# Kernel optimization log

Measured on AMD Instinct MI355X. Metric: run time of the kernel, lower is better.

## Reference

```python
import jax, jax.numpy as jnp
import numpy as np
import math

D = 512  # feature dim (must equal Lv for the final bmm)

def setup_inputs() -> dict:
    key = jax.random.key(0)
    k1, k2, k3 = jax.random.split(key, 3)
    B, Lp, Lq, Lv = 32, 1024, 1024, 512
    linear_pre = jax.random.normal(k1, (B, Lp, D), dtype=jnp.float32)
    linear_q = jax.random.normal(k2, (B, Lq, D), dtype=jnp.float32)
    linear_v = jax.random.normal(k3, (B, Lv, D), dtype=jnp.float32)
    return {"linear_pre": linear_pre, "linear_q": linear_q, "linear_v": linear_v}

def reference(linear_pre, linear_q, linear_v):
    scale = 1.0 / math.sqrt(D)
    # Two parallel softmax-attention streams (exp / sum == softmax over last dim).
    # attnp: [B, Lp, Lq], attne: [B, Lq, Lv]
    attnp = jax.nn.softmax(jnp.einsum('bpd,bqd->bpq', linear_pre, linear_q) * scale, axis=-1)
    attne = jax.nn.softmax(jnp.einsum('bqd,bvd->bqv', linear_q, linear_v) * scale, axis=-1)
    # dropout is identity in eval mode (deterministic reference)
    precompute = jnp.einsum('bpq,bqd->bpd', attnp, linear_q)   # [B, Lp, D]
    energy = jnp.einsum('bqv,bvd->bqd', attne, linear_v)       # [B, Lq, D]
    # final bmm requires D == Lv
    weightedContext = jnp.einsum('bqv,bvd->bqd', energy, linear_v)  # [B, Lq, D]
    return (weightedContext, energy, precompute)
```

## Files before the change

### kernel.cpp

```cpp
#include <hip/hip_runtime.h>

#define BATCH 32
#define LP 1024
#define LQ 1024
#define LV 512
#define DIM 512

typedef __bf16 bf16x8 __attribute__((ext_vector_type(8)));
typedef float f32x4 __attribute__((ext_vector_type(4)));
typedef unsigned short ushort_t;
typedef unsigned short us8 __attribute__((ext_vector_type(8)));

__device__ __forceinline__ ushort_t f2bf(float f) {
  unsigned int u = __float_as_uint(f);
  unsigned int r = (u + 0x7FFFu + ((u >> 16) & 1u)) >> 16;
  return (ushort_t)r;
}

__device__ __forceinline__ void async16(const void* g, void* l) {
  __builtin_amdgcn_global_load_lds(
      (const __attribute__((address_space(1))) unsigned int*)g,
      (__attribute__((address_space(3))) unsigned int*)l, 16, 0, 0);
}

#define BARRIER() asm volatile("s_barrier" ::: "memory")
#define VMCNT(n) asm volatile("s_waitcnt vmcnt(" #n ")" ::: "memory")

__global__ __launch_bounds__(256)
void cvt_kernel(const float* __restrict__ in, ushort_t* __restrict__ out) {
  int i = blockIdx.x * blockDim.x + threadIdx.x;
  const float4* p = (const float4*)in;
  float4 a = p[i * 2], b = p[i * 2 + 1];
  us8 h;
  h[0] = f2bf(a.x); h[1] = f2bf(a.y); h[2] = f2bf(a.z); h[3] = f2bf(a.w);
  h[4] = f2bf(b.x); h[5] = f2bf(b.y); h[6] = f2bf(b.z); h[7] = f2bf(b.w);
  *(us8*)&out[(size_t)i * 8] = h;
}

__global__ void transpose_cvt(const float* __restrict__ in, ushort_t* __restrict__ outT,
                              ushort_t* __restrict__ outR, int R, int C) {
  __shared__ ushort_t tile[32][33];
  int b = blockIdx.z;
  int c0 = blockIdx.x * 32, r0 = blockIdx.y * 32;
  const float* inb = in + (size_t)b * R * C;
  ushort_t* outTb = outT + (size_t)b * R * C;
  ushort_t* outRb = outR + (size_t)b * R * C;
  int x = threadIdx.x, y = threadIdx.y;
#pragma unroll
  for (int k = 0; k < 4; ++k) {
    int r = r0 + y + k * 8;
    ushort_t h = f2bf(inb[(size_t)r * C + c0 + x]);
    tile[y + k * 8][x] = h;
    outRb[(size_t)r * C + c0 + x] = h;
  }
  __syncthreads();
#pragma unroll
  for (int k = 0; k < 4; ++k) {
    int c = c0 + y + k * 8;
    outTb[(size_t)c * R + r0 + x] = tile[x][y + k * 8];
  }
}

template <int H>
__device__ __forceinline__ void mm8(f32x4 (&acc)[8][4], const bf16x8 (&af)[4],
                                    const bf16x8 (&bfv)[4]) {
  __builtin_amdgcn_s_setprio(1);
#pragma unroll
  for (int i = 0; i < 4; ++i)
#pragma unroll
    for (int j = 0; j < 4; ++j)
      acc[H * 4 + i][j] =
          __builtin_amdgcn_mfma_f32_16x16x32_bf16(af[i], bfv[j], acc[H * 4 + i][j], 0, 0, 0);
  __builtin_amdgcn_s_setprio(0);
}

template <int MODE, bool OUT2>
__global__ __launch_bounds__(512, 2)
void gemm256(const ushort_t* __restrict__ A, const ushort_t* __restrict__ BT,
             const float* __restrict__ lsumIn, float* __restrict__ outF,
             ushort_t* __restrict__ outB, float* __restrict__ lsumOut,
             int M, int N, int K) {
  extern __shared__ ushort_t smem[];
  ushort_t* sA = smem;
  ushort_t* sB = smem + 32768;

  int b = blockIdx.z;
  int m0 = blockIdx.x * 256, n0 = blockIdx.y * 256;
  const ushort_t* Ab = A + ((size_t)b * M + m0) * K;
  const ushort_t* Bb = BT + ((size_t)b * N + n0) * K;
  int tid = threadIdx.x;
  int l = tid & 63, w = tid >> 6;
  int wm = w >> 2, wn = w & 3;
  int low = l & 15, quad = l >> 4;
  const int colsw = (quad * 8) ^ ((l & 8) ? 16 : 0);

  int NT = K >> 6;

  f32x4 acc[8][4];
  f32x4 zero = {0.f, 0.f, 0.f, 0.f};
#pragma unroll
  for (int i = 0; i < 8; ++i)
#pragma unroll
    for (int j = 0; j < 4; ++j) acc[i][j] = zero;

  auto stageT = [&](const ushort_t* gb, ushort_t* sbase, int T, int kh) {
    ushort_t* hb = sbase + (((T & 1) << 1) + kh) * 8192;
    int kc0 = (T << 6) + (kh << 5);
#pragma unroll
    for (int ii = 0; ii < 2; ++ii) {
      int o = w * 128 + ii * 64;
      int ol = o + l;
      int cc = ((ol & 3) ^ ((l >> 4) & 2)) << 3;
      async16(gb + (size_t)(ol >> 2) * K + kc0 + cc, hb + o * 8);
    }
  };
  auto ldA = [&](bf16x8 (&af)[4], int buf, int k, int h) {
    const ushort_t* base = sA + ((buf << 1) + k) * 8192 + colsw;
    int r0 = wm * 128 + h * 64 + low;
#pragma unroll
    for (int i = 0; i < 4; ++i) af[i] = *(const bf16x8*)&base[(r0 + i * 16) * 32];
  };
  auto ldB = [&](bf16x8 (&bfv)[4], int buf, int k) {
    const ushort_t* base = sB + ((buf << 1) + k) * 8192 + colsw;
    int r0 = wn * 64 + low;
#pragma unroll
    for (int j = 0; j < 4; ++j) bfv[j] = *(const bf16x8*)&base[(r0 + j * 16) * 32];
  };

  stageT(Ab, sA, 0, 0);
  stageT(Bb, sB, 0, 0);
  stageT(Ab, sA, 0, 1);
  stageT(Bb, sB, 0, 1);
  VMCNT(4);
  if (NT > 1) {
    stageT(Bb, sB, 1, 0);
    stageT(Ab, sA, 1, 0);
    stageT(Bb, sB, 1, 1);
    VMCNT(6);
  } else {
    VMCNT(0);
  }
  BARRIER();

  bf16x8 af[4], bfv[4];
  for (int T = 0; T < NT; ++T) {
    int buf = T & 1;
    ldB(bfv, buf, 0);
    ldA(af, buf, 0, 0);
    if (T + 1 < NT) stageT(Ab, sA, T + 1, 1);
    BARRIER();
    mm8<0>(acc, af, bfv);
    BARRIER();
    ldA(af, buf, 0, 1);
    if (T + 2 < NT) stageT(Bb, sB, T + 2, 0);
    BARRIER();
    mm8<1>(acc, af, bfv);
    BARRIER();
    ldB(bfv, buf, 1);
    ldA(af, buf, 1, 0);
    if (T + 2 < NT) stageT(Ab, sA, T + 2, 0);
    BARRIER();
    mm8<0>(acc, af, bfv);
    BARRIER();
    ldA(af, buf, 1, 1);
    if (T + 2 < NT) stageT(Bb, sB, T + 2, 1);
    if (T + 1 < NT) {
      if (T + 2 < NT) { VMCNT(6); } else { VMCNT(0); }
    }
    BARRIER();
    mm8<1>(acc, af, bfv);
    BARRIER();
  }

  size_t ob = (size_t)b * M * N;
  if (MODE == 2) {
    const float sc = 0.04419417382415922f;
#pragma unroll
    for (int i = 0; i < 8; ++i) {
      int gr0 = m0 + wm * 128 + i * 16 + quad * 4;
#pragma unroll
      for (int r = 0; r < 4; ++r) {
        int gr = gr0 + r;
        float rs = 0.f;
#pragma unroll
        for (int j = 0; j < 4; ++j) {
          float p = __expf(acc[i][j][r] * sc);
          rs += p;
          int gc = n0 + wn * 64 + j * 16 + low;
          outB[ob + (size_t)gr * N + gc] = f2bf(p);
        }
        rs += __shfl_xor(rs, 1);
        rs += __shfl_xor(rs, 2);
        rs += __shfl_xor(rs, 4);
        rs += __shfl_xor(rs, 8);
        if (low == 0) atomicAdd(&lsumOut[(size_t)b * M + gr], rs);
      }
    }
  } else {
#pragma unroll
    for (int i = 0; i < 8; ++i) {
      int gr0 = m0 + wm * 128 + i * 16 + quad * 4;
#pragma unroll
      for (int r = 0; r < 4; ++r) {
        int gr = gr0 + r;
        float inv = 1.f;
        if (MODE == 1) inv = 1.f / lsumIn[(size_t)b * M + gr];
#pragma unroll
        for (int j = 0; j < 4; ++j) {
          int gc = n0 + wn * 64 + j * 16 + low;
          float o = acc[i][j][r] * inv;
          outF[ob + (size_t)gr * N + gc] = o;
          if (OUT2) outB[ob + (size_t)gr * N + gc] = f2bf(o);
        }
      }
    }
  }
}

#define LDS_BYTES 131072

extern "C" void kernel_launch(void* const* d_in, const int* in_sizes, int n_in,
                              void* d_out, int out_size, void* d_ws, size_t ws_size,
                              hipStream_t stream) {
  (void)in_sizes; (void)n_in; (void)out_size; (void)ws_size;
  const float* pre = (const float*)d_in[0];
  const float* q   = (const float*)d_in[1];
  const float* v   = (const float*)d_in[2];

  float* out      = (float*)d_out;
  float* wc       = out;
  float* energy   = out + (size_t)BATCH * LQ * DIM;
  float* precomp  = out + 2 * (size_t)BATCH * LQ * DIM;

  char* ws = (char*)d_ws;
  size_t off = 0;
  auto alloc = [&](size_t bytes) {
    void* p = ws + off;
    off += (bytes + 255) & ~(size_t)255;
    return p;
  };
  ushort_t* preB = (ushort_t*)alloc((size_t)BATCH * LP * DIM * 2);
  ushort_t* qB   = (ushort_t*)alloc((size_t)BATCH * LQ * DIM * 2);
  ushort_t* vB   = (ushort_t*)alloc((size_t)BATCH * LV * DIM * 2);
  ushort_t* qT   = (ushort_t*)alloc((size_t)BATCH * DIM * LQ * 2);
  ushort_t* vT   = (ushort_t*)alloc((size_t)BATCH * DIM * LV * 2);
  ushort_t* Pp   = (ushort_t*)alloc((size_t)BATCH * LP * LQ * 2);
  ushort_t* Pe   = (ushort_t*)alloc((size_t)BATCH * LQ * LV * 2);
  ushort_t* Ebf  = (ushort_t*)alloc((size_t)BATCH * LQ * DIM * 2);
  float* lp = (float*)alloc((size_t)BATCH * LP * 4);
  float* le = (float*)alloc((size_t)BATCH * LQ * 4);

  static bool attr_done = false;
  if (!attr_done) {
    attr_done = true;
    hipFuncSetAttribute(reinterpret_cast<const void*>(&gemm256<2, false>),
                        hipFuncAttributeMaxDynamicSharedMemorySize, LDS_BYTES);
    hipFuncSetAttribute(reinterpret_cast<const void*>(&gemm256<1, false>),
                        hipFuncAttributeMaxDynamicSharedMemorySize, LDS_BYTES);
    hipFuncSetAttribute(reinterpret_cast<const void*>(&gemm256<1, true>),
                        hipFuncAttributeMaxDynamicSharedMemorySize, LDS_BYTES);
    hipFuncSetAttribute(reinterpret_cast<const void*>(&gemm256<0, false>),
                        hipFuncAttributeMaxDynamicSharedMemorySize, LDS_BYTES);
  }

  hipMemsetAsync(lp, 0, (size_t)BATCH * (LP + LQ) * 4, stream);

  cvt_kernel<<<(size_t)BATCH * LP * DIM / 8 / 256, 256, 0, stream>>>(pre, preB);
  transpose_cvt<<<dim3(DIM / 32, LQ / 32, BATCH), dim3(32, 8), 0, stream>>>(q, qT, qB, LQ, DIM);
  transpose_cvt<<<dim3(DIM / 32, LV / 32, BATCH), dim3(32, 8), 0, stream>>>(v, vT, vB, LV, DIM);

  gemm256<2, false><<<dim3(LP / 256, LQ / 256, BATCH), 512, LDS_BYTES, stream>>>(
      preB, qB, nullptr, nullptr, Pp, lp, LP, LQ, DIM);
  gemm256<2, false><<<dim3(LQ / 256, LV / 256, BATCH), 512, LDS_BYTES, stream>>>(
      qB, vB, nullptr, nullptr, Pe, le, LQ, LV, DIM);

  gemm256<1, false><<<dim3(LP / 256, DIM / 256, BATCH), 512, LDS_BYTES, stream>>>(
      Pp, qT, lp, precomp, nullptr, nullptr, LP, DIM, LQ);
  gemm256<1, true><<<dim3(LQ / 256, DIM / 256, BATCH), 512, LDS_BYTES, stream>>>(
      Pe, vT, le, energy, Ebf, nullptr, LQ, DIM, LV);
  gemm256<0, false><<<dim3(LQ / 256, DIM / 256, BATCH), 512, LDS_BYTES, stream>>>(
      Ebf, vT, nullptr, wc, nullptr, nullptr, LQ, DIM, LV);
}
```

Measured before the change: 530.8 us.

## Merge independent GEMMs into grouped launches and fuse input prep kernels

Replaces the three conversion and transpose kernels with a single prep kernel that uses 64x64 tiles and vectorized loads and stores. The GEMM template is turned into a runtime-parameterized kernel taking two segment descriptors, so the two independent score GEMMs share one launch and the two PV GEMMs share another. A block-index swizzle interleaves batches across groups of eight. This is meant to cut launch count and tail idle time and to improve L2 locality. In exchange the mode is chosen at runtime instead of at compile time, which may add register pressure or branching in the epilogue.

```diff
diff --git a/kernel.cpp b/kernel.cpp
--- a/kernel.cpp
+++ b/kernel.cpp
@@ -10,6 +10,7 @@
 typedef float f32x4 __attribute__((ext_vector_type(4)));
 typedef unsigned short ushort_t;
 typedef unsigned short us8 __attribute__((ext_vector_type(8)));
+typedef unsigned short us4 __attribute__((ext_vector_type(4)));
 
 __device__ __forceinline__ ushort_t f2bf(float f) {
   unsigned int u = __float_as_uint(f);
@@ -27,37 +28,53 @@
 #define VMCNT(n) asm volatile("s_waitcnt vmcnt(" #n ")" ::: "memory")
 
 __global__ __launch_bounds__(256)
-void cvt_kernel(const float* __restrict__ in, ushort_t* __restrict__ out) {
-  int i = blockIdx.x * blockDim.x + threadIdx.x;
-  const float4* p = (const float4*)in;
-  float4 a = p[i * 2], b = p[i * 2 + 1];
-  us8 h;
-  h[0] = f2bf(a.x); h[1] = f2bf(a.y); h[2] = f2bf(a.z); h[3] = f2bf(a.w);
-  h[4] = f2bf(b.x); h[5] = f2bf(b.y); h[6] = f2bf(b.z); h[7] = f2bf(b.w);
-  *(us8*)&out[(size_t)i * 8] = h;
-}
-
-__global__ void transpose_cvt(const float* __restrict__ in, ushort_t* __restrict__ outT,
-                              ushort_t* __restrict__ outR, int R, int C) {
-  __shared__ ushort_t tile[32][33];
-  int b = blockIdx.z;
-  int c0 = blockIdx.x * 32, r0 = blockIdx.y * 32;
-  const float* inb = in + (size_t)b * R * C;
-  ushort_t* outTb = outT + (size_t)b * R * C;
-  ushort_t* outRb = outR + (size_t)b * R * C;
-  int x = threadIdx.x, y = threadIdx.y;
+void prep_kernel(const float* __restrict__ pre, const float* __restrict__ q,
+                 const float* __restrict__ v, ushort_t* __restrict__ preB,
+                 ushort_t* __restrict__ qB, ushort_t* __restrict__ vB,
+                 ushort_t* __restrict__ qT, ushort_t* __restrict__ vT) {
+  __shared__ ushort_t tile[64][68];
+  int fid = blockIdx.x, tid = threadIdx.x;
+
+  if (fid < 8192) {
+    size_t i = (size_t)fid * 256 + tid;
+    const float4* p = (const float4*)pre;
+    float4 a = p[i * 2], b = p[i * 2 + 1];
+    us8 h;
+    h[0] = f2bf(a.x); h[1] = f2bf(a.y); h[2] = f2bf(a.z); h[3] = f2bf(a.w);
+    h[4] = f2bf(b.x); h[5] = f2bf(b.y); h[6] = f2bf(b.z); h[7] = f2bf(b.w);
+    *(us8*)&preB[i * 8] = h;
+    return;
+  }
+
+  int lid; const float* in; ushort_t* oT; ushort_t* oR; int R;
+  if (fid < 12288) { lid = fid - 8192;  in = q; oT = qT; oR = qB; R = LQ; }
+  else             { lid = fid - 12288; in = v; oT = vT; oR = vB; R = LV; }
+  int tiles = (R / 64) * (DIM / 64);
+  int b = lid / tiles, t = lid % tiles;
+  int r0 = (t / (DIM / 64)) * 64, c0 = (t % (DIM / 64)) * 64;
+  const float* ib = in + (size_t)b * R * DIM;
+  ushort_t* oRb = oR + (size_t)b * R * DIM;
+  ushort_t* oTb = oT + (size_t)b * R * DIM;
+
+  int rr = tid >> 4, c4 = (tid & 15) << 2;
 #pragma unroll
   for (int k = 0; k < 4; ++k) {
-    int r = r0 + y + k * 8;
-    ushort_t h = f2bf(inb[(size_t)r * C + c0 + x]);
-    tile[y + k * 8][x] = h;
-    outRb[(size_t)r * C + c0 + x] = h;
+    int r = rr + k * 16;
+    float4 f = *(const float4*)&ib[(size_t)(r0 + r) * DIM + c0 + c4];
+    us4 o;
+    o[0] = f2bf(f.x); o[1] = f2bf(f.y); o[2] = f2bf(f.z); o[3] = f2bf(f.w);
+    *(us4*)&tile[r][c4] = o;
+    *(us4*)&oRb[(size_t)(r0 + r) * DIM + c0 + c4] = o;
   }
   __syncthreads();
 #pragma unroll
-  for (int k = 0; k < 4; ++k) {
-    int c = c0 + y + k * 8;
-    outTb[(size_t)c * R + r0 + x] = tile[x][y + k * 8];
+  for (int j = 0; j < 2; ++j) {
+    int idx = tid + 256 * j;
+    int c = idx >> 3, r8 = (idx & 7) << 3;
+    us8 o;
+#pragma unroll
+    for (int i = 0; i < 8; ++i) o[i] = tile[r8 + i][c];
+    *(us8*)&oTb[(size_t)(c0 + c) * R + r0 + r8] = o;
   }
 }
 
@@ -74,26 +91,42 @@
   __builtin_amdgcn_s_setprio(0);
 }
 
-template <int MODE, bool OUT2>
+struct GSeg {
+  const ushort_t* A;
+  const ushort_t* BT;
+  const float* lsumIn;
+  float* outF;
+  ushort_t* outB;
+  float* lsumOut;
+  int M, N, K, gx, gy, nblk, mode;
+};
+
 __global__ __launch_bounds__(512, 2)
-void gemm256(const ushort_t* __restrict__ A, const ushort_t* __restrict__ BT,
-             const float* __restrict__ lsumIn, float* __restrict__ outF,
-             ushort_t* __restrict__ outB, float* __restrict__ lsumOut,
-             int M, int N, int K) {
+void gemm256d(GSeg s0, GSeg s1, int split) {
   extern __shared__ ushort_t smem[];
   ushort_t* sA = smem;
   ushort_t* sB = smem + 32768;
 
-  int b = blockIdx.z;
-  int m0 = blockIdx.x * 256, n0 = blockIdx.y * 256;
-  const ushort_t* Ab = A + ((size_t)b * M + m0) * K;
-  const ushort_t* Bb = BT + ((size_t)b * N + n0) * K;
+  int fid = blockIdx.x;
+  bool second = fid >= split;
+  GSeg s = second ? s1 : s0;
+  int lid = second ? fid - split : fid;
+  int cpx = s.nblk >> 3;
+  int swz = (lid & 7) * cpx + (lid >> 3);
+  int x = swz % s.gx;
+  int t = swz / s.gx;
+  int y = t % s.gy;
+  int b = t / s.gy;
+
+  int m0 = x * 256, n0 = y * 256;
+  const ushort_t* Ab = s.A + ((size_t)b * s.M + m0) * s.K;
+  const ushort_t* Bb = s.BT + ((size_t)b * s.N + n0) * s.K;
   int tid = threadIdx.x;
   int l = tid & 63, w = tid >> 6;
   int wm = w >> 2, wn = w & 3;
   int low = l & 15, quad = l >> 4;
   const int colsw = (quad * 8) ^ ((l & 8) ? 16 : 0);
-
+  const int K = s.K;
   int NT = K >> 6;
 
   f32x4 acc[8][4];
@@ -172,8 +205,8 @@
     BARRIER();
   }
 
-  size_t ob = (size_t)b * M * N;
-  if (MODE == 2) {
+  size_t ob = (size_t)b * s.M * s.N;
+  if (s.mode == 2) {
     const float sc = 0.04419417382415922f;
 #pragma unroll
     for (int i = 0; i < 8; ++i) {
@@ -187,13 +220,13 @@
           float p = __expf(acc[i][j][r] * sc);
           rs += p;
           int gc = n0 + wn * 64 + j * 16 + low;
-          outB[ob + (size_t)gr * N + gc] = f2bf(p);
+          s.outB[ob + (size_t)gr * s.N + gc] = f2bf(p);
         }
         rs += __shfl_xor(rs, 1);
         rs += __shfl_xor(rs, 2);
         rs += __shfl_xor(rs, 4);
         rs += __shfl_xor(rs, 8);
-        if (low == 0) atomicAdd(&lsumOut[(size_t)b * M + gr], rs);
+        if (low == 0) atomicAdd(&s.lsumOut[(size_t)b * s.M + gr], rs);
       }
     }
   } else {
@@ -204,13 +237,13 @@
       for (int r = 0; r < 4; ++r) {
         int gr = gr0 + r;
         float inv = 1.f;
-        if (MODE == 1) inv = 1.f / lsumIn[(size_t)b * M + gr];
+        if (s.lsumIn) inv = 1.f / s.lsumIn[(size_t)b * s.M + gr];
 #pragma unroll
         for (int j = 0; j < 4; ++j) {
           int gc = n0 + wn * 64 + j * 16 + low;
           float o = acc[i][j][r] * inv;
-          outF[ob + (size_t)gr * N + gc] = o;
-          if (OUT2) outB[ob + (size_t)gr * N + gc] = f2bf(o);
+          s.outF[ob + (size_t)gr * s.N + gc] = o;
+          if (s.outB) s.outB[ob + (size_t)gr * s.N + gc] = f2bf(o);
         }
       }
     }
@@ -253,31 +286,27 @@
   static bool attr_done = false;
   if (!attr_done) {
     attr_done = true;
-    hipFuncSetAttribute(reinterpret_cast<const void*>(&gemm256<2, false>),
+    hipFuncSetAttribute(reinterpret_cast<const void*>(&gemm256d),
                         hipFuncAttributeMaxDynamicSharedMemorySize, LDS_BYTES);
-    hipFuncSetAttribute(reinterpret_cast<const void*>(&gemm256<1, false>),
-                        hipFuncAttributeMaxDynamicSharedMemorySize, LDS_BYTES);
-    hipFuncSetAttribute(reinterpret_cast<const void*>(&gemm256<1, true>),
-                        hipFuncAttributeMaxDynamicSharedMemorySize, LDS_BYTES);
-    hipFuncSetAttribute(reinterpret_cast<const void*>(&gemm256<0, false>),
-                        hipFuncAttributeMaxDynamicSharedMemorySize, LDS_BYTES);
   }
 
   hipMemsetAsync(lp, 0, (size_t)BATCH * (LP + LQ) * 4, stream);
 
-  cvt_kernel<<<(size_t)BATCH * LP * DIM / 8 / 256, 256, 0, stream>>>(pre, preB);
-  transpose_cvt<<<dim3(DIM / 32, LQ / 32, BATCH), dim3(32, 8), 0, stream>>>(q, qT, qB, LQ, DIM);
-  transpose_cvt<<<dim3(DIM / 32, LV / 32, BATCH), dim3(32, 8), 0, stream>>>(v, vT, vB, LV, DIM);
-
-  gemm256<2, false><<<dim3(LP / 256, LQ / 256, BATCH), 512, LDS_BYTES, stream>>>(
-      preB, qB, nullptr, nullptr, Pp, lp, LP, LQ, DIM);
-  gemm256<2, false><<<dim3(LQ / 256, LV / 256, BATCH), 512, LDS_BYTES, stream>>>(
-      qB, vB, nullptr, nullptr, Pe, le, LQ, LV, DIM);
-
-  gemm256<1, false><<<dim3(LP / 256, DIM / 256, BATCH), 512, LDS_BYTES, stream>>>(
-      Pp, qT, lp, precomp, nullptr, nullptr, LP, DIM, LQ);
-  gemm256<1, true><<<dim3(LQ / 256, DIM / 256, BATCH), 512, LDS_BYTES, stream>>>(
-      Pe, vT, le, energy, Ebf, nullptr, LQ, DIM, LV);
-  gemm256<0, false><<<dim3(LQ / 256, DIM / 256, BATCH), 512, LDS_BYTES, stream>>>(
-      Ebf, vT, nullptr, wc, nullptr, nullptr, LQ, DIM, LV);
-}
+  prep_kernel<<<8192 + 4096 + 2048, 256, 0, stream>>>(pre, q, v, preB, qB, vB, qT, vT);
+
+  GSeg sc1 = {preB, qB, nullptr, nullptr, Pp, lp, LP, LQ, DIM, LP / 256, LQ / 256,
+              (LP / 256) * (LQ / 256) * BATCH, 2};
+  GSeg sc2 = {qB, vB, nullptr, nullptr, Pe, le, LQ, LV, DIM, LQ / 256, LV / 256,
+              (LQ / 256) * (LV / 256) * BATCH, 2};
+  gemm256d<<<sc1.nblk + sc2.nblk, 512, LDS_BYTES, stream>>>(sc1, sc2, sc1.nblk);
+
+  GSeg pv1 = {Pp, qT, lp, precomp, nullptr, nullptr, LP, DIM, LQ, LP / 256, DIM / 256,
+              (LP / 256) * (DIM / 256) * BATCH, 1};
+  GSeg pv2 = {Pe, vT, le, energy, Ebf, nullptr, LQ, DIM, LV, LQ / 256, DIM / 256,
+              (LQ / 256) * (DIM / 256) * BATCH, 1};
+  gemm256d<<<pv1.nblk + pv2.nblk, 512, LDS_BYTES, stream>>>(pv1, pv2, pv1.nblk);
+
+  GSeg wcs = {Ebf, vT, nullptr, wc, nullptr, nullptr, LQ, DIM, LV, LQ / 256, DIM / 256,
+              (LQ / 256) * (DIM / 256) * BATCH, 0};
+  gemm256d<<<wcs.nblk, 512, LDS_BYTES, stream>>>(wcs, wcs, wcs.nblk);
+}
```

Result: faster. 505.0 us (-4.9%).
